# Kernel tuning notes

Measured on AMD Instinct MI355X. Metric: run time of the kernel, lower is better.

Reference implementation:

```python
import jax, jax.numpy as jnp
import numpy as np

GN_EPS = 1e-5

def setup_inputs() -> dict:
    key = jax.random.key(0)
    k1, k2, k3, k4 = jax.random.split(key, 4)
    B, N, C, O, H, W = 1024, 64, 768, 768, 8, 8
    FW = W // 2 + 1
    return {
        "spatial_tokens": jax.random.normal(k1, (B, N, C), dtype=jnp.float32),
        "weight_real": jax.random.normal(k2, (1, C, H, FW), dtype=jnp.float32),
        "weight_imag": jax.random.normal(k3, (1, C, H, FW), dtype=jnp.float32),
        "proj_w": jax.random.normal(k4, (O, C), dtype=jnp.float32) * (1.0 / np.sqrt(C)),
        "gn_w": jnp.ones((O,), dtype=jnp.float32),
        "gn_b": jnp.zeros((O,), dtype=jnp.float32),
        "h_feat": H,
        "w_feat": W,
    }

def reference(spatial_tokens, weight_real, weight_imag, proj_w, gn_w, gn_b, h_feat, w_feat):
    B, N, C = spatial_tokens.shape
    # (B, N, C) -> (B, C, H, W)
    x = spatial_tokens.transpose(0, 2, 1).reshape(B, C, h_feat, w_feat)
    # Learnable complex bandpass in rfft2 domain (ortho norm)
    x_freq = jnp.fft.rfft2(x, norm="ortho")  # (B, C, H, W//2+1)
    x_freq = x_freq * (weight_real + 1j * weight_imag)
    x_enh = jnp.fft.irfft2(x_freq, s=(h_feat, w_feat), norm="ortho")  # (B, C, H, W)
    # 1x1 conv (no bias)
    y = jnp.einsum("bchw,oc->bohw", x_enh, proj_w)  # (B, O, H, W)
    # GroupNorm(num_groups=1): normalize over (C,H,W) per sample, biased variance
    mean = jnp.mean(y, axis=(1, 2, 3), keepdims=True)
    var = jnp.var(y, axis=(1, 2, 3), keepdims=True)
    y = (y - mean) * jax.lax.rsqrt(var + GN_EPS)
    y = y * gn_w[None, :, None, None] + gn_b[None, :, None, None]
    # Exact GELU (torch nn.GELU default)
    y = jax.nn.gelu(y, approximate=False)
    # (B, O, H, W) -> (B, N, O)
    return y.reshape(B, -1, h_feat * w_feat).transpose(0, 2, 1)
```

## Files before the change

### kernel.cpp

```cpp
#include <hip/hip_runtime.h>
#include <cstddef>

typedef __attribute__((ext_vector_type(4))) float  float4v;
typedef __attribute__((ext_vector_type(8))) short  short8v;
typedef __attribute__((ext_vector_type(8))) unsigned short ushort8v;
typedef __attribute__((ext_vector_type(8))) __bf16 bf16x8;
typedef __attribute__((ext_vector_type(4))) float  f32x4;

static constexpr int C_DIM = 768;
static constexpr int O_DIM = 768;
static constexpr int NEL   = 49152;

__device__ __forceinline__ unsigned short f2bf(float f) {
  unsigned u = __builtin_bit_cast(unsigned, f);
  u += 0x7FFFu + ((u >> 16) & 1u);
  return (unsigned short)(u >> 16);
}

__device__ __forceinline__ void rfft8p(float& x0, float& x1, float& x2, float& x3,
                                       float& x4, float& x5, float& x6, float& x7) {
  const float Cc = 0.70710678118654752f;
  float b0 = x0 + x4, b1 = x1 + x5, b2 = x2 + x6, b3 = x3 + x7;
  float d0 = x0 - x4, d1 = x1 - x5, d2 = x2 - x6, d3 = x3 - x7;
  float e0 = b0 + b2, e1 = b1 + b3, f0 = b0 - b2, f1 = b1 - b3;
  float t1 = Cc * (d1 - d3), t2 = Cc * (d1 + d3);
  x0 = e0 + e1; x4 = e0 - e1;
  x2 = f0;      x6 = -f1;
  x1 = d0 + t1; x7 = -(t2 + d2);
  x3 = d0 - t1; x5 = d2 - t2;
}

__device__ __forceinline__ void irfft8p(float& x0, float& x1, float& x2, float& x3,
                                        float& x4, float& x5, float& x6, float& x7) {
  const float Cc = 0.70710678118654752f;
  float R0 = x0, R1 = x1, R2 = x2, R3 = x3, R4 = x4, I3 = x5, I2 = x6, I1 = x7;
  float p = R0 + R4, q = R0 - R4;
  float u = 2.f * R2, vv = 2.f * I2;
  float g1 = R1 + R3, g2 = R1 - R3, g3 = I1 + I3, g4 = I1 - I3;
  float E1 = p + u, E2 = p - u;
  float B1 = 2.f * g1, B2 = 2.f * g4;
  float A1 = 2.f * Cc * (g2 - g3), A2c_ = 2.f * Cc * (g2 + g3);
  x0 = E1 + B1;  x4 = E1 - B1;
  x2 = E2 - B2;  x6 = E2 + B2;
  x1 = q + A1 - vv;  x5 = q - A1 - vv;
  x3 = q - A2c_ + vv;  x7 = q + A2c_ + vv;
}

template<bool INV>
__device__ __forceinline__ void cfft8(
    float& r0, float& r1, float& r2, float& r3, float& r4, float& r5, float& r6, float& r7,
    float& i0, float& i1, float& i2, float& i3, float& i4, float& i5, float& i6, float& i7) {
  const float Cc = 0.70710678118654752f;
  float s0r = r0 + r4, s0i = i0 + i4, s1r = r2 + r6, s1i = i2 + i6;
  float t0r = r0 - r4, t0i = i0 - i4, t1r = r2 - r6, t1i = i2 - i6;
  float E0r = s0r + s1r, E0i = s0i + s1i;
  float E2r = s0r - s1r, E2i = s0i - s1i;
  float E1r, E1i, E3r, E3i;
  if (!INV) { E1r = t0r + t1i; E1i = t0i - t1r; E3r = t0r - t1i; E3i = t0i + t1r; }
  else      { E1r = t0r - t1i; E1i = t0i + t1r; E3r = t0r + t1i; E3i = t0i - t1r; }
  float u0r = r1 + r5, u0i = i1 + i5, u1r = r3 + r7, u1i = i3 + i7;
  float p0r = r1 - r5, p0i = i1 - i5, p1r = r3 - r7, p1i = i3 - i7;
  float O0r = u0r + u1r, O0i = u0i + u1i;
  float O2r = u0r - u1r, O2i = u0i - u1i;
  float O1r, O1i, O3r, O3i;
  if (!INV) { O1r = p0r + p1i; O1i = p0i - p1r; O3r = p0r - p1i; O3i = p0i + p1r; }
  else      { O1r = p0r - p1i; O1i = p0i + p1r; O3r = p0r + p1i; O3i = p0i - p1r; }
  float W1r, W1i, W2r, W2i, W3r, W3i;
  if (!INV) {
    W1r = Cc * (O1r + O1i); W1i = Cc * (O1i - O1r);
    W2r = O2i;              W2i = -O2r;
    W3r = Cc * (O3i - O3r); W3i = -Cc * (O3r + O3i);
  } else {
    W1r = Cc * (O1r - O1i); W1i = Cc * (O1i + O1r);
    W2r = -O2i;             W2i = O2r;
    W3r = -Cc * (O3r + O3i); W3i = Cc * (O3r - O3i);
  }
  r0 = E0r + O0r; i0 = E0i + O0i;  r4 = E0r - O0r; i4 = E0i - O0i;
  r1 = E1r + W1r; i1 = E1i + W1i;  r5 = E1r - W1r; i5 = E1i - W1i;
  r2 = E2r + W2r; i2 = E2i + W2i;  r6 = E2r - W2r; i6 = E2i - W2i;
  r3 = E3r + W3r; i3 = E3i + W3i;  r7 = E3r - W3r; i7 = E3i - W3i;
}

__global__ __launch_bounds__(256) void k_convert_proj(const float* __restrict__ p,
                                                      unsigned short* __restrict__ pb) {
  int t = blockIdx.x * 256 + threadIdx.x;
  int o = t / 96, cb = t - o * 96;
  const float* src = p + o * 768 + cb * 8;
  float4v v0 = *(const float4v*)(src);
  float4v v1 = *(const float4v*)(src + 4);
  ushort8v w;
#pragma unroll
  for (int r = 0; r < 4; ++r) { w[r] = f2bf(v0[r]); w[r + 4] = f2bf(v1[r]); }
  int ks = cb >> 2, g = cb & 3;
  int nf = o >> 4, l15 = o & 15;
  size_t off = ((size_t)(ks * 48 + nf) * 64 + g * 16 + l15) * 8;
  *(ushort8v*)(pb + off) = w;
}

__global__ __launch_bounds__(256) void k_prep_w(const float* __restrict__ wre,
                                                const float* __restrict__ wim,
                                                float* __restrict__ wT0,
                                                float* __restrict__ wT1) {
  int i = blockIdx.x * 256 + threadIdx.x;
  if (i >= 40 * 768) return;
  int k = i / 768, c = i - k * 768;
  int h = k / 5, w = k - h * 5;
  const float S = 1.0f / 64.0f;
  const float* wr = wre + c * 40;
  const float* wi = wim + c * 40;
  float ar, ai;
  if (w == 0 || w == 4) {
    if (h == 0 || h == 4)      { ar = wr[k] * S; ai = 0.f; }
    else if (h <= 3)           { ar = (wr[h * 5 + w] + wr[(8 - h) * 5 + w]) * (0.5f * S);
                                 ai = (wi[h * 5 + w] - wi[(8 - h) * 5 + w]) * (0.5f * S); }
    else                       { ar = 0.f; ai = 0.f; }
  } else                       { ar = wr[k] * S; ai = wi[k] * S; }
  wT0[i] = ar; wT1[i] = ai;
}

__device__ __forceinline__ float gelu_fast(float x) {
  float p = x * x;
  float q = fmaf(p, -0.1029434f, -2.3022082f);
  float e = exp2f(x * q);
  return x * __builtin_amdgcn_rcpf(1.0f + e);
}

__device__ __forceinline__ void fft_tile(const float* __restrict__ xb, int c,
                                         const float* __restrict__ wT0,
                                         const float* __restrict__ wT1,
                                         unsigned short* A2) {
  float v[8][8];
#pragma unroll
  for (int m = 0; m < 8; ++m)
#pragma unroll
    for (int n = 0; n < 8; ++n) v[m][n] = xb[(m * 8 + n) * C_DIM + c];

#define ROWV(m) v[m][0], v[m][1], v[m][2], v[m][3], v[m][4], v[m][5], v[m][6], v[m][7]
#define COLV(w) v[0][w], v[1][w], v[2][w], v[3][w], v[4][w], v[5][w], v[6][w], v[7][w]
#pragma unroll
  for (int m = 0; m < 8; ++m) rfft8p(ROWV(m));
  rfft8p(COLV(0));
  rfft8p(COLV(4));
  cfft8<false>(COLV(1), COLV(7));
  cfft8<false>(COLV(2), COLV(6));
  cfft8<false>(COLV(3), COLV(5));

#define LR(k) wT0[(k) * 768 + c]
#define LI(k) wT1[(k) * 768 + c]
#pragma unroll
  for (int w = 0; w <= 4; w += 4) {
    v[0][w] *= LR(w);
    v[4][w] *= LR(20 + w);
#pragma unroll
    for (int h = 1; h <= 3; ++h) {
      float ar = LR(h * 5 + w), ai = LI(h * 5 + w);
      float re = v[h][w], im = v[8 - h][w];
      v[h][w]     = re * ar - im * ai;
      v[8 - h][w] = re * ai + im * ar;
    }
  }
#pragma unroll
  for (int w = 1; w <= 3; ++w) {
#pragma unroll
    for (int h = 0; h < 8; ++h) {
      float ar = LR(h * 5 + w), ai = LI(h * 5 + w);
      float re = v[h][w], im = v[h][8 - w];
      v[h][w]     = re * ar - im * ai;
      v[h][8 - w] = re * ai + im * ar;
    }
  }
#undef LR
#undef LI

  irfft8p(COLV(0));
  irfft8p(COLV(4));
  cfft8<true>(COLV(1), COLV(7));
  cfft8<true>(COLV(2), COLV(6));
  cfft8<true>(COLV(3), COLV(5));
#pragma unroll
  for (int m = 0; m < 8; ++m) irfft8p(ROWV(m));
#undef ROWV
#undef COLV

  char* base = (char*)A2;
#pragma unroll
  for (int m = 0; m < 8; ++m)
#pragma unroll
    for (int n = 0; n < 8; ++n) {
      const int hw = m * 8 + n;
      int off = (hw * 1536 + c * 2) ^ ((hw & 7) << 4);
      *(unsigned short*)(base + off) = f2bf(v[m][n]);
    }
}

__global__ __launch_bounds__(512, 2) void k_fused(const float* __restrict__ x,
                                                  const float* __restrict__ wT0,
                                                  const float* __restrict__ wT1,
                                                  const unsigned short* __restrict__ projB,
                                                  const float* __restrict__ gnw,
                                                  const float* __restrict__ gnb,
                                                  float* __restrict__ out) {
  __shared__ __align__(16) unsigned short A2[64 * 768];
  __shared__ float redS[8], redQ[8];

  const int b    = blockIdx.x;
  const int tid  = threadIdx.x;
  const int wid  = tid >> 6;
  const int lane = tid & 63;
  const int g    = lane >> 4;
  const int l15  = lane & 15;

  const unsigned short* Bb = projB + ((size_t)(wid * 6) * 64 + lane) * 8;

#define LOADB(BF, KS)                                                        \
  do {                                                                       \
    _Pragma("unroll") for (int nf = 0; nf < 6; ++nf)                         \
        BF[nf] = *(const short8v*)&Bb[(KS) * 24576 + nf * 512];              \
  } while (0)

  short8v a0[4], b0[6], a1[4], b1[6], a2[4], b2[6];
  LOADB(b0, 0);
  LOADB(b1, 1);

  const float* xb = x + (size_t)b * NEL;
  fft_tile(xb, tid, wT0, wT1, A2);
  if (tid < 256) fft_tile(xb, 512 + tid, wT0, wT1, A2);
  __syncthreads();

  const char* A2c = (const char*)A2;
  const int swz = (l15 & 7) << 4;

#define LOADA(AF, KS)                                                        \
  do {                                                                       \
    _Pragma("unroll") for (int mf = 0; mf < 4; ++mf)                         \
        AF[mf] = *(const short8v*)(A2c +                                     \
            (((mf * 16 + l15) * 1536 + (KS) * 64 + g * 16) ^ swz));          \
  } while (0)

#define MFMAS(AF, BF)                                                        \
  do {                                                                       \
    _Pragma("unroll") for (int mf = 0; mf < 4; ++mf)                         \
        _Pragma("unroll") for (int nf = 0; nf < 6; ++nf)                     \
            acc[mf][nf] = __builtin_amdgcn_mfma_f32_16x16x32_bf16(           \
                __builtin_bit_cast(bf16x8, AF[mf]), __builtin_bit_cast(bf16x8, BF[nf]),\
                acc[mf][nf], 0, 0, 0);                                       \
  } while (0)

  f32x4 acc[4][6];
#pragma unroll
  for (int mf = 0; mf < 4; ++mf)
#pragma unroll
    for (int nf = 0; nf < 6; ++nf) acc[mf][nf] = f32x4{0.f, 0.f, 0.f, 0.f};

  LOADA(a0, 0);
  LOADA(a1, 1);
#pragma unroll 1
  for (int ks = 0; ks < 21; ks += 3) {
    LOADB(b2, ks + 2); LOADA(a2, ks + 2);
    MFMAS(a0, b0);
    LOADB(b0, ks + 3); LOADA(a0, ks + 3);
    MFMAS(a1, b1);
    LOADB(b1, ks + 4); LOADA(a1, ks + 4);
    MFMAS(a2, b2);
  }
  LOADB(b2, 23); LOADA(a2, 23);
  MFMAS(a0, b0);
  MFMAS(a1, b1);
  MFMAS(a2, b2);

  float s = 0.f, ss = 0.f;
#pragma unroll
  for (int mf = 0; mf < 4; ++mf)
#pragma unroll
    for (int nf = 0; nf < 6; ++nf)
#pragma unroll
      for (int r = 0; r < 4; ++r) {
        float t = acc[mf][nf][r];
        s += t;
        ss += t * t;
      }
#pragma unroll
  for (int off = 32; off > 0; off >>= 1) {
    s  += __shfl_xor(s, off, 64);
    ss += __shfl_xor(ss, off, 64);
  }
  if (lane == 0) { redS[wid] = s; redQ[wid] = ss; }
  __syncthreads();
  float Stot = 0.f, Qtot = 0.f;
#pragma unroll
  for (int i = 0; i < 8; ++i) { Stot += redS[i]; Qtot += redQ[i]; }
  constexpr float invN = 1.0f / 49152.0f;
  const float mean = Stot * invN;
  const float inv  = rsqrtf(fmaxf(Qtot * invN - mean * mean, 0.f) + 1e-5f);

  float* outb = out + (size_t)b * NEL;
#pragma unroll
  for (int nf = 0; nf < 6; ++nf) {
    const int o = wid * 96 + nf * 16 + l15;
    const float gw = gnw[o], gb_ = gnb[o];
#pragma unroll
    for (int mf = 0; mf < 4; ++mf)
#pragma unroll
      for (int r = 0; r < 4; ++r) {
        const int hw = mf * 16 + g * 4 + r;
        float t = (acc[mf][nf][r] - mean) * inv;
        t = t * gw + gb_;
        outb[(size_t)hw * O_DIM + o] = gelu_fast(t);
      }
  }
#undef LOADA
#undef LOADB
#undef MFMAS
}

extern "C" void kernel_launch(void* const* d_in, const int* in_sizes, int n_in,
                              void* d_out, int out_size, void* d_ws, size_t ws_size,
                              hipStream_t stream) {
  const float* x   = (const float*)d_in[0];
  const float* wre = (const float*)d_in[1];
  const float* wim = (const float*)d_in[2];
  const float* pw  = (const float*)d_in[3];
  const float* gnw = (const float*)d_in[4];
  const float* gnb = (const float*)d_in[5];
  float* out = (float*)d_out;

  const int B = in_sizes[0] / NEL;

  unsigned short* projB = (unsigned short*)d_ws;
  float* wT0 = (float*)((char*)d_ws + (2u << 20));
  float* wT1 = (float*)((char*)d_ws + (2u << 20) + (256u << 10));

  k_convert_proj<<<288, 256, 0, stream>>>(pw, projB);
  k_prep_w<<<120, 256, 0, stream>>>(wre, wim, wT0, wT1);
  k_fused<<<B, 512, 0, stream>>>(x, wT0, wT1, projB, gnw, gnb, out);
}
```

Baseline: 173.6 us.

## Make fused kernel persistent with 1024-thread blocks splitting output columns

The fused FFT+GEMM+GroupNorm kernel becomes a persistent 256-block kernel that loops over batch samples. Each block now has 1024 threads, so each of 16 waves computes 48 output channels instead of 96. The three A buffers shrink to one reloaded register set, and the reduction scratch is double-buffered to avoid a race across iterations. This trims per-wave register pressure and launch overhead, but it gives up the overlap of FFT and GEMM phases between two co-resident blocks. It also doubles LDS reads of the A operand.

```diff
diff --git a/kernel.cpp b/kernel.cpp
--- a/kernel.cpp
+++ b/kernel.cpp
@@ -193,42 +193,31 @@
     }
 }
 
-__global__ __launch_bounds__(512, 2) void k_fused(const float* __restrict__ x,
-                                                  const float* __restrict__ wT0,
-                                                  const float* __restrict__ wT1,
-                                                  const unsigned short* __restrict__ projB,
-                                                  const float* __restrict__ gnw,
-                                                  const float* __restrict__ gnb,
-                                                  float* __restrict__ out) {
+__global__ __launch_bounds__(1024) void k_fused(const float* __restrict__ x,
+                                                const float* __restrict__ wT0,
+                                                const float* __restrict__ wT1,
+                                                const unsigned short* __restrict__ projB,
+                                                const float* __restrict__ gnw,
+                                                const float* __restrict__ gnb,
+                                                float* __restrict__ out, int B) {
   __shared__ __align__(16) unsigned short A2[64 * 768];
-  __shared__ float redS[8], redQ[8];
-
-  const int b    = blockIdx.x;
+  __shared__ float redS[2][16], redQ[2][16];
+
   const int tid  = threadIdx.x;
   const int wid  = tid >> 6;
   const int lane = tid & 63;
   const int g    = lane >> 4;
   const int l15  = lane & 15;
 
-  const unsigned short* Bb = projB + ((size_t)(wid * 6) * 64 + lane) * 8;
+  const unsigned short* Bb = projB + ((size_t)(wid * 3) * 64 + lane) * 8;
+  const char* A2c = (const char*)A2;
+  const int swz = (l15 & 7) << 4;
 
 #define LOADB(BF, KS)                                                        \
   do {                                                                       \
-    _Pragma("unroll") for (int nf = 0; nf < 6; ++nf)                         \
+    _Pragma("unroll") for (int nf = 0; nf < 3; ++nf)                         \
         BF[nf] = *(const short8v*)&Bb[(KS) * 24576 + nf * 512];              \
   } while (0)
-
-  short8v a0[4], b0[6], a1[4], b1[6], a2[4], b2[6];
-  LOADB(b0, 0);
-  LOADB(b1, 1);
-
-  const float* xb = x + (size_t)b * NEL;
-  fft_tile(xb, tid, wT0, wT1, A2);
-  if (tid < 256) fft_tile(xb, 512 + tid, wT0, wT1, A2);
-  __syncthreads();
-
-  const char* A2c = (const char*)A2;
-  const int swz = (l15 & 7) << 4;
 
 #define LOADA(AF, KS)                                                        \
   do {                                                                       \
@@ -240,73 +229,83 @@
 #define MFMAS(AF, BF)                                                        \
   do {                                                                       \
     _Pragma("unroll") for (int mf = 0; mf < 4; ++mf)                         \
-        _Pragma("unroll") for (int nf = 0; nf < 6; ++nf)                     \
+        _Pragma("unroll") for (int nf = 0; nf < 3; ++nf)                     \
             acc[mf][nf] = __builtin_amdgcn_mfma_f32_16x16x32_bf16(           \
                 __builtin_bit_cast(bf16x8, AF[mf]), __builtin_bit_cast(bf16x8, BF[nf]),\
                 acc[mf][nf], 0, 0, 0);                                       \
   } while (0)
 
-  f32x4 acc[4][6];
-#pragma unroll
-  for (int mf = 0; mf < 4; ++mf)
-#pragma unroll
-    for (int nf = 0; nf < 6; ++nf) acc[mf][nf] = f32x4{0.f, 0.f, 0.f, 0.f};
-
-  LOADA(a0, 0);
-  LOADA(a1, 1);
+  int par = 0;
+  for (int b = blockIdx.x; b < B; b += gridDim.x) {
+    short8v b0[3], b1[3], b2[3], aR[4];
+    LOADB(b0, 0);
+    LOADB(b1, 1);
+
+    const float* xb = x + (size_t)b * NEL;
+    if (tid < 768) fft_tile(xb, tid, wT0, wT1, A2);
+    __syncthreads();
+
+    f32x4 acc[4][3];
+#pragma unroll
+    for (int mf = 0; mf < 4; ++mf)
+#pragma unroll
+      for (int nf = 0; nf < 3; ++nf) acc[mf][nf] = f32x4{0.f, 0.f, 0.f, 0.f};
+
 #pragma unroll 1
-  for (int ks = 0; ks < 21; ks += 3) {
-    LOADB(b2, ks + 2); LOADA(a2, ks + 2);
-    MFMAS(a0, b0);
-    LOADB(b0, ks + 3); LOADA(a0, ks + 3);
-    MFMAS(a1, b1);
-    LOADB(b1, ks + 4); LOADA(a1, ks + 4);
-    MFMAS(a2, b2);
-  }
-  LOADB(b2, 23); LOADA(a2, 23);
-  MFMAS(a0, b0);
-  MFMAS(a1, b1);
-  MFMAS(a2, b2);
-
-  float s = 0.f, ss = 0.f;
-#pragma unroll
-  for (int mf = 0; mf < 4; ++mf)
-#pragma unroll
-    for (int nf = 0; nf < 6; ++nf)
-#pragma unroll
-      for (int r = 0; r < 4; ++r) {
-        float t = acc[mf][nf][r];
-        s += t;
-        ss += t * t;
-      }
-#pragma unroll
-  for (int off = 32; off > 0; off >>= 1) {
-    s  += __shfl_xor(s, off, 64);
-    ss += __shfl_xor(ss, off, 64);
-  }
-  if (lane == 0) { redS[wid] = s; redQ[wid] = ss; }
-  __syncthreads();
-  float Stot = 0.f, Qtot = 0.f;
-#pragma unroll
-  for (int i = 0; i < 8; ++i) { Stot += redS[i]; Qtot += redQ[i]; }
-  constexpr float invN = 1.0f / 49152.0f;
-  const float mean = Stot * invN;
-  const float inv  = rsqrtf(fmaxf(Qtot * invN - mean * mean, 0.f) + 1e-5f);
-
-  float* outb = out + (size_t)b * NEL;
-#pragma unroll
-  for (int nf = 0; nf < 6; ++nf) {
-    const int o = wid * 96 + nf * 16 + l15;
-    const float gw = gnw[o], gb_ = gnb[o];
+    for (int ks = 0; ks < 21; ks += 3) {
+      LOADB(b2, ks + 2);
+      LOADA(aR, ks);     MFMAS(aR, b0);
+      LOADB(b0, ks + 3);
+      LOADA(aR, ks + 1); MFMAS(aR, b1);
+      LOADB(b1, ks + 4);
+      LOADA(aR, ks + 2); MFMAS(aR, b2);
+    }
+    LOADB(b2, 23);
+    LOADA(aR, 21); MFMAS(aR, b0);
+    LOADA(aR, 22); MFMAS(aR, b1);
+    LOADA(aR, 23); MFMAS(aR, b2);
+
+    float s = 0.f, ss = 0.f;
 #pragma unroll
     for (int mf = 0; mf < 4; ++mf)
 #pragma unroll
-      for (int r = 0; r < 4; ++r) {
-        const int hw = mf * 16 + g * 4 + r;
-        float t = (acc[mf][nf][r] - mean) * inv;
-        t = t * gw + gb_;
-        outb[(size_t)hw * O_DIM + o] = gelu_fast(t);
-      }
+      for (int nf = 0; nf < 3; ++nf)
+#pragma unroll
+        for (int r = 0; r < 4; ++r) {
+          float t = acc[mf][nf][r];
+          s += t;
+          ss += t * t;
+        }
+#pragma unroll
+    for (int off = 32; off > 0; off >>= 1) {
+      s  += __shfl_xor(s, off, 64);
+      ss += __shfl_xor(ss, off, 64);
+    }
+    if (lane == 0) { redS[par][wid] = s; redQ[par][wid] = ss; }
+    __syncthreads();
+    float Stot = 0.f, Qtot = 0.f;
+#pragma unroll
+    for (int i = 0; i < 16; ++i) { Stot += redS[par][i]; Qtot += redQ[par][i]; }
+    constexpr float invN = 1.0f / 49152.0f;
+    const float mean = Stot * invN;
+    const float inv  = rsqrtf(fmaxf(Qtot * invN - mean * mean, 0.f) + 1e-5f);
+
+    float* outb = out + (size_t)b * NEL;
+#pragma unroll
+    for (int nf = 0; nf < 3; ++nf) {
+      const int o = wid * 48 + nf * 16 + l15;
+      const float gw = gnw[o], gb_ = gnb[o];
+#pragma unroll
+      for (int mf = 0; mf < 4; ++mf)
+#pragma unroll
+        for (int r = 0; r < 4; ++r) {
+          const int hw = mf * 16 + g * 4 + r;
+          float t = (acc[mf][nf][r] - mean) * inv;
+          t = t * gw + gb_;
+          outb[(size_t)hw * O_DIM + o] = gelu_fast(t);
+        }
+    }
+    par ^= 1;
   }
 #undef LOADA
 #undef LOADB
@@ -332,5 +331,5 @@
 
   k_convert_proj<<<288, 256, 0, stream>>>(pw, projB);
   k_prep_w<<<120, 256, 0, stream>>>(wre, wim, wT0, wT1);
-  k_fused<<<B, 512, 0, stream>>>(x, wT0, wT1, projB, gnw, gnb, out);
-}
+  k_fused<<<256, 1024, 0, stream>>>(x, wT0, wT1, projB, gnw, gnb, out, B);
+}
```

Measured after the change: 537.2 us. 210% more time.

## Split channel dimension into two halves to halve LDS tile and reuse buffer

Applied to the files above, without the earlier changes.

The FFT stage now processes channels in two chunks of 384, writing into a half-size LDS buffer, with the GEMM over K split into two phases separated by barriers. This halves shared memory per block, which can allow more resident blocks or waves, and drops two of the A-fragment register buffers to reduce register pressure. The cost is extra synchronisation and serialisation: FFT and MFMA phases no longer overlap within a block, and only 384 of 512 threads do FFT work. The bf16 conversion now uses the compiler's native cast instead of manual rounding.

```diff
diff --git a/kernel.cpp b/kernel.cpp
--- a/kernel.cpp
+++ b/kernel.cpp
@@ -12,9 +12,8 @@
 static constexpr int NEL   = 49152;
 
 __device__ __forceinline__ unsigned short f2bf(float f) {
-  unsigned u = __builtin_bit_cast(unsigned, f);
-  u += 0x7FFFu + ((u >> 16) & 1u);
-  return (unsigned short)(u >> 16);
+  __bf16 h = (__bf16)f;
+  return __builtin_bit_cast(unsigned short, h);
 }
 
 __device__ __forceinline__ void rfft8p(float& x0, float& x1, float& x2, float& x3,
@@ -125,7 +124,7 @@
   return x * __builtin_amdgcn_rcpf(1.0f + e);
 }
 
-__device__ __forceinline__ void fft_tile(const float* __restrict__ xb, int c,
+__device__ __forceinline__ void fft_tile(const float* __restrict__ xb, int c, int lc,
                                          const float* __restrict__ wT0,
                                          const float* __restrict__ wT1,
                                          unsigned short* A2) {
@@ -188,7 +187,7 @@
 #pragma unroll
     for (int n = 0; n < 8; ++n) {
       const int hw = m * 8 + n;
-      int off = (hw * 1536 + c * 2) ^ ((hw & 7) << 4);
+      int off = (hw * 768 + lc * 2) ^ ((hw & 7) << 4);
       *(unsigned short*)(base + off) = f2bf(v[m][n]);
     }
 }
@@ -200,7 +199,7 @@
                                                   const float* __restrict__ gnw,
                                                   const float* __restrict__ gnb,
                                                   float* __restrict__ out) {
-  __shared__ __align__(16) unsigned short A2[64 * 768];
+  __shared__ __align__(16) unsigned short A2[64 * 384];
   __shared__ float redS[8], redQ[8];
 
   const int b    = blockIdx.x;
@@ -211,6 +210,9 @@
   const int l15  = lane & 15;
 
   const unsigned short* Bb = projB + ((size_t)(wid * 6) * 64 + lane) * 8;
+  const char* A2c = (const char*)A2;
+  const int swz = (l15 & 7) << 4;
+  const float* xb = x + (size_t)b * NEL;
 
 #define LOADB(BF, KS)                                                        \
   do {                                                                       \
@@ -218,23 +220,11 @@
         BF[nf] = *(const short8v*)&Bb[(KS) * 24576 + nf * 512];              \
   } while (0)
 
-  short8v a0[4], b0[6], a1[4], b1[6], a2[4], b2[6];
-  LOADB(b0, 0);
-  LOADB(b1, 1);
-
-  const float* xb = x + (size_t)b * NEL;
-  fft_tile(xb, tid, wT0, wT1, A2);
-  if (tid < 256) fft_tile(xb, 512 + tid, wT0, wT1, A2);
-  __syncthreads();
-
-  const char* A2c = (const char*)A2;
-  const int swz = (l15 & 7) << 4;
-
 #define LOADA(AF, KS)                                                        \
   do {                                                                       \
     _Pragma("unroll") for (int mf = 0; mf < 4; ++mf)                         \
         AF[mf] = *(const short8v*)(A2c +                                     \
-            (((mf * 16 + l15) * 1536 + (KS) * 64 + g * 16) ^ swz));          \
+            (((mf * 16 + l15) * 768 + (KS) * 64 + g * 16) ^ swz));           \
   } while (0)
 
 #define MFMAS(AF, BF)                                                        \
@@ -246,27 +236,44 @@
                 acc[mf][nf], 0, 0, 0);                                       \
   } while (0)
 
+  short8v b0[6], b1[6], b2[6], aR[4];
+
+  LOADB(b0, 0);
+
+  if (tid < 384) fft_tile(xb, tid, tid, wT0, wT1, A2);
+  __syncthreads();
+
   f32x4 acc[4][6];
 #pragma unroll
   for (int mf = 0; mf < 4; ++mf)
 #pragma unroll
     for (int nf = 0; nf < 6; ++nf) acc[mf][nf] = f32x4{0.f, 0.f, 0.f, 0.f};
 
-  LOADA(a0, 0);
-  LOADA(a1, 1);
+  LOADB(b1, 1);
 #pragma unroll 1
-  for (int ks = 0; ks < 21; ks += 3) {
-    LOADB(b2, ks + 2); LOADA(a2, ks + 2);
-    MFMAS(a0, b0);
-    LOADB(b0, ks + 3); LOADA(a0, ks + 3);
-    MFMAS(a1, b1);
-    LOADB(b1, ks + 4); LOADA(a1, ks + 4);
-    MFMAS(a2, b2);
-  }
-  LOADB(b2, 23); LOADA(a2, 23);
-  MFMAS(a0, b0);
-  MFMAS(a1, b1);
-  MFMAS(a2, b2);
+  for (int ks = 0; ks < 9; ks += 3) {
+    LOADB(b2, ks + 2); LOADA(aR, ks);     MFMAS(aR, b0);
+    LOADB(b0, ks + 3); LOADA(aR, ks + 1); MFMAS(aR, b1);
+    LOADB(b1, ks + 4); LOADA(aR, ks + 2); MFMAS(aR, b2);
+  }
+  LOADB(b2, 11); LOADA(aR, 9);  MFMAS(aR, b0);
+  LOADB(b0, 12); LOADA(aR, 10); MFMAS(aR, b1);
+  LOADA(aR, 11); MFMAS(aR, b2);
+  __syncthreads();
+
+  if (tid < 384) fft_tile(xb, 384 + tid, tid, wT0, wT1, A2);
+  __syncthreads();
+
+  LOADB(b1, 13);
+#pragma unroll 1
+  for (int ks = 0; ks < 9; ks += 3) {
+    LOADB(b2, ks + 14); LOADA(aR, ks);     MFMAS(aR, b0);
+    LOADB(b0, ks + 15); LOADA(aR, ks + 1); MFMAS(aR, b1);
+    LOADB(b1, ks + 16); LOADA(aR, ks + 2); MFMAS(aR, b2);
+  }
+  LOADB(b2, 23); LOADA(aR, 9);  MFMAS(aR, b0);
+  LOADA(aR, 10); MFMAS(aR, b1);
+  LOADA(aR, 11); MFMAS(aR, b2);
 
   float s = 0.f, ss = 0.f;
 #pragma unroll
```

Result: no change. 176.2 us (+1.5%).
